# Performance work log

Hardware: AMD Instinct MI355X
Metric: run time of the kernel (lower is better)

The kernel has to match this reference:

```python
import jax, jax.numpy as jnp
import numpy as np

B, G, D = 16, 20000, 64   # batch, num_genes, feature_dim
S, L = 500, 128           # num_gene_sets, max genes per set (padded)


def setup_inputs() -> dict:
    key = jax.random.key(0)
    k1, k2, k3 = jax.random.split(key, 3)
    gene_features = jax.random.normal(k1, (B, G, D), dtype=jnp.float32)
    geneset_indices = jax.random.randint(k2, (S, L), 0, G, dtype=jnp.int32)
    set_mask = jnp.ones((S, L), dtype=bool)  # all positions valid (uniform-size sets)
    attn_weights = jax.random.normal(k3, (S, L, D), dtype=jnp.float32)
    return {
        "gene_features": gene_features,
        "attn_weights": attn_weights,
        "geneset_indices": geneset_indices,
        "set_mask": set_mask,
    }


def reference(gene_features, attn_weights, geneset_indices, set_mask):
    # Gather per-set gene features: [B, S, L, D]
    gathered = jnp.take(gene_features, geneset_indices, axis=1)
    # Masked softmax over the set-member axis L (independent per feature dim),
    # matching F.softmax(attention_weights, dim=1) per gene set.
    neg = jnp.finfo(attn_weights.dtype).min
    logits = jnp.where(set_mask[:, :, None], attn_weights, neg)  # [S, L, D]
    attn = jax.nn.softmax(logits, axis=1)                        # [S, L, D]
    # Weighted sum over set members -> [B, S, D]
    return jnp.einsum('bsld,sld->bsd', gathered, attn)
```

## Files before the change

### kernel.cpp

```cpp
#include <hip/hip_runtime.h>
#include <math.h>


#define NB 16
#define NG 20000
#define ND 64
#define NS 500
#define NL 128

__device__ __forceinline__ float bf2f(unsigned short u) {
    union { unsigned int i; float f; } x;
    x.i = ((unsigned int)u) << 16;
    return x.f;
}

__device__ __forceinline__ unsigned short f2bf(float f) {
    union { float f; unsigned int i; } x;
    x.f = f;
    unsigned int r = x.i + 0x7FFFu + ((x.i >> 16) & 1u);
    return (unsigned short)(r >> 16);
}

__global__ void detect_dtype_kernel(const unsigned short* __restrict__ aw,
                                    int* __restrict__ flag) {
    const unsigned int e = ((unsigned int)aw[2 * threadIdx.x] >> 7) & 0xFFu;
    const unsigned long long m = __ballot(e >= 100u && e <= 135u);
    if (threadIdx.x == 0) *flag = (__popcll(m) >= 32) ? 1 : 0;
}

template<bool BF16>
__global__ __launch_bounds__(1024)
void agg_kernel(const void* __restrict__ gf_,
                const void* __restrict__ aw_,
                const int*  __restrict__ idx,
                void*       __restrict__ out_,
                const int*  __restrict__ flag)
{
    if (*flag != (BF16 ? 1 : 0)) return;

    __shared__ float attn_s[NL * ND];
    __shared__ float red[16 * ND];
    __shared__ float inv_sum[ND];
    __shared__ int   gidx[NL];
    __shared__ float part_red[4 * 16 * 16 * 4];

    const int s = blockIdx.x;
    const int t = threadIdx.x;

    if (t < NL) gidx[t] = idx[s * NL + t];

    const int d    = t & 63;
    const int part = t >> 6;
    const unsigned short* awp = (const unsigned short*)aw_ + (size_t)s * (NL * ND);

    float m = -INFINITY;
    #pragma unroll
    for (int i = 0; i < 8; ++i) {
        const int l = part * 8 + i;
        const float v = BF16 ? bf2f(awp[l * ND + d])
                             : ((const float*)aw_)[(size_t)s * (NL * ND) + l * ND + d];
        attn_s[l * ND + d] = v;
        m = fmaxf(m, v);
    }
    red[part * ND + d] = m;
    __syncthreads();
    float m_all = -INFINITY;
    #pragma unroll
    for (int p = 0; p < 16; ++p) m_all = fmaxf(m_all, red[p * ND + d]);
    __syncthreads();

    float psum = 0.f;
    #pragma unroll
    for (int i = 0; i < 8; ++i) {
        const int l = part * 8 + i;
        const float e = __expf(attn_s[l * ND + d] - m_all);
        attn_s[l * ND + d] = e;
        psum += e;
    }
    red[part * ND + d] = psum;
    __syncthreads();
    if (part == 0) {
        float tot = 0.f;
        #pragma unroll
        for (int p = 0; p < 16; ++p) tot += red[p * ND + d];
        inv_sum[d] = 1.0f / tot;
    }
    __syncthreads();

    const int q  = t & 15;
    const int bl = (t >> 4) & 15;
    const int lp = t >> 8;
    const int d0 = q * 4;

    float ax = 0.f, ay = 0.f, az = 0.f, aww = 0.f;
    if (BF16) {
        const unsigned short* gbase = (const unsigned short*)gf_ + (size_t)bl * (NG * ND) + d0;
        #pragma unroll 4
        for (int k = 0; k < 32; ++k) {
            const int l = lp * 32 + k;
            const int g = gidx[l];
            const ushort4 u = *(const ushort4*)(gbase + (size_t)g * ND);
            const float4  w = *(const float4*)&attn_s[l * ND + d0];
            ax  += bf2f(u.x) * w.x;
            ay  += bf2f(u.y) * w.y;
            az  += bf2f(u.z) * w.z;
            aww += bf2f(u.w) * w.w;
        }
    } else {
        const float* gbase = (const float*)gf_ + (size_t)bl * (NG * ND) + d0;
        #pragma unroll 4
        for (int k = 0; k < 32; ++k) {
            const int l = lp * 32 + k;
            const int g = gidx[l];
            const float4 u = *(const float4*)(gbase + (size_t)g * ND);
            const float4 w = *(const float4*)&attn_s[l * ND + d0];
            ax  += u.x * w.x;
            ay  += u.y * w.y;
            az  += u.z * w.z;
            aww += u.w * w.w;
        }
    }

    float* pr = &part_red[((lp * 16 + bl) * 16 + q) * 4];
    pr[0] = ax; pr[1] = ay; pr[2] = az; pr[3] = aww;
    __syncthreads();

    if (lp == 0) {
        float r0 = 0.f, r1 = 0.f, r2 = 0.f, r3 = 0.f;
        #pragma unroll
        for (int p = 0; p < 4; ++p) {
            const float4 v = *(const float4*)&part_red[((p * 16 + bl) * 16 + q) * 4];
            r0 += v.x; r1 += v.y; r2 += v.z; r3 += v.w;
        }
        r0 *= inv_sum[d0 + 0];
        r1 *= inv_sum[d0 + 1];
        r2 *= inv_sum[d0 + 2];
        r3 *= inv_sum[d0 + 3];
        if (BF16) {
            ushort4 o;
            o.x = f2bf(r0); o.y = f2bf(r1); o.z = f2bf(r2); o.w = f2bf(r3);
            *(ushort4*)((unsigned short*)out_ + ((size_t)bl * NS + s) * ND + d0) = o;
        } else {
            float4 o; o.x = r0; o.y = r1; o.z = r2; o.w = r3;
            *(float4*)((float*)out_ + ((size_t)bl * NS + s) * ND + d0) = o;
        }
    }
}

extern "C" void kernel_launch(void* const* d_in, const int* in_sizes, int n_in,
                              void* d_out, int out_size, void* d_ws, size_t ws_size,
                              hipStream_t stream) {
    const void* gf  = d_in[0];
    const void* aw  = d_in[1];
    const int*  idx = (const int*)d_in[2];
    int* flag = (int*)d_ws;

    detect_dtype_kernel<<<1, 64, 0, stream>>>((const unsigned short*)aw, flag);
    agg_kernel<true ><<<NS, 1024, 0, stream>>>(gf, aw, idx, d_out, flag);
    agg_kernel<false><<<NS, 1024, 0, stream>>>(gf, aw, idx, d_out, flag);
}
```

Baseline: 152.2 us.

## Transpose bf16 gene features to gene-major layout before gathered aggregation

Adds a pre-pass that rewrites bf16 gene_features from [B,G,D] into a gene-major [G,B,D] workspace buffer. Each gathered gene then becomes one contiguous 2 KB read covering all batches instead of 16 scattered 128-byte reads. The new aggregation kernel unpacks bf16 pairs with bit ops and reduces partial sums through shared-memory atomics. The cost is an extra full pass over the feature tensor every call, plus a dependency on workspace size; when the workspace is too small the old path is kept.

```diff
diff --git a/kernel.cpp b/kernel.cpp
--- a/kernel.cpp
+++ b/kernel.cpp
@@ -21,6 +21,15 @@
     return (unsigned short)(r >> 16);
 }
 
+__device__ __forceinline__ void acc2(float& alo, float& ahi, unsigned int u,
+                                     float wlo, float whi) {
+    union { unsigned int i; float f; } lo, hi;
+    lo.i = u << 16;
+    hi.i = u & 0xFFFF0000u;
+    alo += lo.f * wlo;
+    ahi += hi.f * whi;
+}
+
 __global__ void detect_dtype_kernel(const unsigned short* __restrict__ aw,
                                     int* __restrict__ flag) {
     const unsigned int e = ((unsigned int)aw[2 * threadIdx.x] >> 7) & 0xFFu;
@@ -28,14 +37,139 @@
     if (threadIdx.x == 0) *flag = (__popcll(m) >= 32) ? 1 : 0;
 }
 
+__global__ __launch_bounds__(1024)
+void transpose_gf_bf16(const unsigned short* __restrict__ gf,
+                       unsigned short* __restrict__ gfT,
+                       const int* __restrict__ flag) {
+    if (*flag != 1) return;
+    const int W    = blockIdx.x * 16 + (threadIdx.x >> 6);
+    const int lane = threadIdx.x & 63;
+    const int bq   = lane >> 3;
+    const int d0   = (lane & 7) * 8;
+    for (int g = W; g < NG; g += 8000) {
+        #pragma unroll
+        for (int h = 0; h < 2; ++h) {
+            const int b = h * 8 + bq;
+            const float4 v = *(const float4*)(gf + (size_t)b * (NG * ND) +
+                                              (size_t)g * ND + d0);
+            *(float4*)(gfT + (size_t)g * (NB * ND) + h * 512 + lane * 8) = v;
+        }
+    }
+}
+
+__global__ __launch_bounds__(1024)
+void agg_t_bf16(const unsigned short* __restrict__ gfT,
+                const unsigned short* __restrict__ aw,
+                const int*            __restrict__ idx,
+                unsigned short*       __restrict__ out,
+                const int*            __restrict__ flag) {
+    if (*flag != 1) return;
+
+    __shared__ float attn_s[NL * ND];
+    __shared__ float red[16 * ND];
+    __shared__ float inv_sum[ND];
+    __shared__ int   gidx[NL];
+    __shared__ float acc_s[NB * 65];
+
+    const int s = blockIdx.x;
+    const int t = threadIdx.x;
+
+    if (t < NL) gidx[t] = idx[s * NL + t];
+    for (int z = t; z < NB * 65; z += 1024) acc_s[z] = 0.f;
+
+    const int d    = t & 63;
+    const int part = t >> 6;
+    const unsigned short* awp = aw + (size_t)s * (NL * ND);
+
+    float m = -INFINITY;
+    #pragma unroll
+    for (int i = 0; i < 8; ++i) {
+        const int l = part * 8 + i;
+        const float v = bf2f(awp[l * ND + d]);
+        attn_s[l * ND + d] = v;
+        m = fmaxf(m, v);
+    }
+    red[part * ND + d] = m;
+    __syncthreads();
+    float m_all = -INFINITY;
+    #pragma unroll
+    for (int p = 0; p < 16; ++p) m_all = fmaxf(m_all, red[p * ND + d]);
+    __syncthreads();
+
+    float psum = 0.f;
+    #pragma unroll
+    for (int i = 0; i < 8; ++i) {
+        const int l = part * 8 + i;
+        const float e = __expf(attn_s[l * ND + d] - m_all);
+        attn_s[l * ND + d] = e;
+        psum += e;
+    }
+    red[part * ND + d] = psum;
+    __syncthreads();
+    if (part == 0) {
+        float tot = 0.f;
+        #pragma unroll
+        for (int p = 0; p < 16; ++p) tot += red[p * ND + d];
+        inv_sum[d] = 1.0f / tot;
+    }
+    __syncthreads();
+
+    const int lane = t & 63;
+    const int w    = t >> 6;
+    const int bq   = lane >> 3;
+    const int d8   = (lane & 7) * 8;
+
+    float a0[8], a1[8];
+    #pragma unroll
+    for (int c = 0; c < 8; ++c) { a0[c] = 0.f; a1[c] = 0.f; }
+
+    #pragma unroll 2
+    for (int j = 0; j < 8; ++j) {
+        const int l = w + 16 * j;
+        const int g = gidx[l];
+        const float4* gp = (const float4*)(gfT + (size_t)g * (NB * ND));
+        const float4 u0 = gp[lane];
+        const float4 u1 = gp[64 + lane];
+        const float4* wp = (const float4*)&attn_s[l * ND + d8];
+        const float4 w0 = wp[0];
+        const float4 w1 = wp[1];
+
+        acc2(a0[0], a0[1], __float_as_uint(u0.x), w0.x, w0.y);
+        acc2(a0[2], a0[3], __float_as_uint(u0.y), w0.z, w0.w);
+        acc2(a0[4], a0[5], __float_as_uint(u0.z), w1.x, w1.y);
+        acc2(a0[6], a0[7], __float_as_uint(u0.w), w1.z, w1.w);
+        acc2(a1[0], a1[1], __float_as_uint(u1.x), w0.x, w0.y);
+        acc2(a1[2], a1[3], __float_as_uint(u1.y), w0.z, w0.w);
+        acc2(a1[4], a1[5], __float_as_uint(u1.z), w1.x, w1.y);
+        acc2(a1[6], a1[7], __float_as_uint(u1.w), w1.z, w1.w);
+    }
+
+    #pragma unroll
+    for (int c = 0; c < 8; ++c) {
+        atomicAdd(&acc_s[bq * 65 + d8 + c], a0[c]);
+        atomicAdd(&acc_s[(bq + 8) * 65 + d8 + c], a1[c]);
+    }
+    __syncthreads();
+
+    if (t < 256) {
+        const int b  = t >> 4;
+        const int d0 = (t & 15) * 4;
+        ushort4 o;
+        o.x = f2bf(acc_s[b * 65 + d0 + 0] * inv_sum[d0 + 0]);
+        o.y = f2bf(acc_s[b * 65 + d0 + 1] * inv_sum[d0 + 1]);
+        o.z = f2bf(acc_s[b * 65 + d0 + 2] * inv_sum[d0 + 2]);
+        o.w = f2bf(acc_s[b * 65 + d0 + 3] * inv_sum[d0 + 3]);
+        *(ushort4*)(out + ((size_t)b * NS + s) * ND + d0) = o;
+    }
+}
+
 template<bool BF16>
 __global__ __launch_bounds__(1024)
-void agg_kernel(const void* __restrict__ gf_,
+void agg_direct(const void* __restrict__ gf_,
                 const void* __restrict__ aw_,
                 const int*  __restrict__ idx,
                 void*       __restrict__ out_,
-                const int*  __restrict__ flag)
-{
+                const int*  __restrict__ flag) {
     if (*flag != (BF16 ? 1 : 0)) return;
 
     __shared__ float attn_s[NL * ND];
@@ -46,7 +180,6 @@
 
     const int s = blockIdx.x;
     const int t = threadIdx.x;
-
     if (t < NL) gidx[t] = idx[s * NL + t];
 
     const int d    = t & 63;
@@ -100,11 +233,11 @@
             const int l = lp * 32 + k;
             const int g = gidx[l];
             const ushort4 u = *(const ushort4*)(gbase + (size_t)g * ND);
-            const float4  w = *(const float4*)&attn_s[l * ND + d0];
-            ax  += bf2f(u.x) * w.x;
-            ay  += bf2f(u.y) * w.y;
-            az  += bf2f(u.z) * w.z;
-            aww += bf2f(u.w) * w.w;
+            const float4  ww = *(const float4*)&attn_s[l * ND + d0];
+            ax  += bf2f(u.x) * ww.x;
+            ay  += bf2f(u.y) * ww.y;
+            az  += bf2f(u.z) * ww.z;
+            aww += bf2f(u.w) * ww.w;
         }
     } else {
         const float* gbase = (const float*)gf_ + (size_t)bl * (NG * ND) + d0;
@@ -113,11 +246,11 @@
             const int l = lp * 32 + k;
             const int g = gidx[l];
             const float4 u = *(const float4*)(gbase + (size_t)g * ND);
-            const float4 w = *(const float4*)&attn_s[l * ND + d0];
-            ax  += u.x * w.x;
-            ay  += u.y * w.y;
-            az  += u.z * w.z;
-            aww += u.w * w.w;
+            const float4 ww = *(const float4*)&attn_s[l * ND + d0];
+            ax  += u.x * ww.x;
+            ay  += u.y * ww.y;
+            az  += u.z * ww.z;
+            aww += u.w * ww.w;
         }
     }
 
@@ -154,8 +287,18 @@
     const void* aw  = d_in[1];
     const int*  idx = (const int*)d_in[2];
     int* flag = (int*)d_ws;
+    unsigned short* gfT = (unsigned short*)((char*)d_ws + 256);
+
+    const size_t need = 256 + (size_t)NG * NB * ND * sizeof(unsigned short);
 
     detect_dtype_kernel<<<1, 64, 0, stream>>>((const unsigned short*)aw, flag);
-    agg_kernel<true ><<<NS, 1024, 0, stream>>>(gf, aw, idx, d_out, flag);
-    agg_kernel<false><<<NS, 1024, 0, stream>>>(gf, aw, idx, d_out, flag);
-}
+    if (ws_size >= need) {
+        transpose_gf_bf16<<<NS, 1024, 0, stream>>>((const unsigned short*)gf, gfT, flag);
+        agg_t_bf16<<<NS, 1024, 0, stream>>>(gfT, (const unsigned short*)aw, idx,
+                                            (unsigned short*)d_out, flag);
+        agg_direct<false><<<NS, 1024, 0, stream>>>(gf, aw, idx, d_out, flag);
+    } else {
+        agg_direct<true ><<<NS, 1024, 0, stream>>>(gf, aw, idx, d_out, flag);
+        agg_direct<false><<<NS, 1024, 0, stream>>>(gf, aw, idx, d_out, flag);
+    }
+}
```

Result: no change. 153.2 us (+0.6%).
